# Performance work log

Measured on AMD Instinct MI355X. Metric: run time of the kernel, lower is better.

The kernel has to match this reference:

```python
import jax, jax.numpy as jnp
import numpy as np

N_NODES = 50000
N_EDGES = 800000
IN_C, HID_C, OUT_C = 128, 128, 64


def gcn_conv(x, src, dst, W, b, n_nodes):
    """PyG GCNConv: add self-loops, symmetric deg^-1/2 normalization,
    linear transform, scatter-add aggregation at target nodes, add bias."""
    # in-degree over (A + I), unit edge weights
    deg = jax.ops.segment_sum(jnp.ones(dst.shape[0], dtype=x.dtype), dst,
                              num_segments=n_nodes)
    dinv = jnp.where(deg > 0, jax.lax.rsqrt(deg), 0.0)
    norm = dinv[src] * dinv[dst]                      # [E+N]
    h = x @ W                                          # [N, out]
    msg = h[src] * norm[:, None]                       # gather + scale
    out = jax.ops.segment_sum(msg, dst, num_segments=n_nodes)  # scatter-add
    return out + b


def setup_inputs() -> dict:
    key = jax.random.key(0)
    k1, k2, k3, k4 = jax.random.split(key, 4)
    x = jax.random.normal(k1, (N_NODES, IN_C), dtype=jnp.float32)
    edge_index = jax.random.randint(k2, (2, N_EDGES), 0, N_NODES, dtype=jnp.int32)
    # Glorot-ish init for weights, zero bias (PyG default bias=True, zeros)
    W1 = jax.random.normal(k3, (IN_C, HID_C), dtype=jnp.float32) * (1.0 / np.sqrt(IN_C))
    b1 = jnp.zeros((HID_C,), dtype=jnp.float32)
    W2 = jax.random.normal(k4, (HID_C, OUT_C), dtype=jnp.float32) * (1.0 / np.sqrt(HID_C))
    b2 = jnp.zeros((OUT_C,), dtype=jnp.float32)
    return {"x": x, "edge_index": edge_index, "W1": W1, "b1": b1, "W2": W2, "b2": b2}


def reference(x, edge_index, W1, b1, W2, b2):
    n_nodes = x.shape[0]
    # add self-loops once (shared by both conv layers)
    loop = jnp.arange(n_nodes, dtype=edge_index.dtype)
    src = jnp.concatenate([edge_index[0], loop])
    dst = jnp.concatenate([edge_index[1], loop])
    h = gcn_conv(x, src, dst, W1, b1, n_nodes)
    h = jax.nn.relu(h)
    out = gcn_conv(h, src, dst, W2, b2, n_nodes)
    return out
```

## Files before the change

### kernel.cpp

```cpp
#include <hip/hip_runtime.h>
#include <hip/hip_fp16.h>


#define N_NODES 50000
#define N_EDGES 800000
#define BINW    128
#define NBIN    391
#define CAP     2560
#define CAP2    6656
#define B_CHUNK 2048
#define NB_SCAT ((N_EDGES + B_CHUNK - 1) / B_CHUNK)

typedef __bf16 bf16x8 __attribute__((ext_vector_type(8)));
typedef float  f32x4  __attribute__((ext_vector_type(4)));

template<int N>
__device__ inline void wprep_body(const float* __restrict__ W,
                                  __bf16* __restrict__ hi, __bf16* __restrict__ lo,
                                  int idx) {
    if (idx >= (N / 16) * 4 * 64) return;
    int l = idx & 63;
    int s = (idx >> 6) & 3;
    int c = idx >> 8;
    int n = c * 16 + (l & 15);
    int k0 = s * 32 + (l >> 4) * 8;
#pragma unroll
    for (int j = 0; j < 8; j++) {
        float w = W[(k0 + j) * N + n];
        __bf16 h = (__bf16)w;
        hi[idx * 8 + j] = h;
        lo[idx * 8 + j] = (__bf16)(w - (float)h);
    }
}

__global__ __launch_bounds__(256) void prep_kernel(
        const float* __restrict__ W1, const float* __restrict__ W2,
        __bf16* __restrict__ w1hi, __bf16* __restrict__ w1lo,
        __bf16* __restrict__ w2hi, __bf16* __restrict__ w2lo,
        int* __restrict__ gcur, __half* __restrict__ hs1, __half* __restrict__ hs2) {
    int b = blockIdx.x, tid = threadIdx.x;
    if (b < 8)       wprep_body<128>(W1, w1hi, w1lo, b * 256 + tid);
    else if (b < 12) wprep_body<64> (W2, w2hi, w2lo, (b - 8) * 256 + tid);
    else {
        for (int i = tid; i < NBIN; i += 256) gcur[i] = 0;
        if (tid < 128) hs1[(size_t)N_NODES * 128 + tid] = __float2half(0.f);
        if (tid < 64)  hs2[(size_t)N_NODES * 64 + tid] = __float2half(0.f);
    }
}


__global__ __launch_bounds__(256) void bin_scatter_kernel(
        const int* __restrict__ src, const int* __restrict__ dst,
        int* __restrict__ gcur, unsigned* __restrict__ ebin) {
    __shared__ int cnt[512];
    __shared__ int boff[512];
    __shared__ int bcur[512];
    __shared__ int gbase[512];
    __shared__ unsigned stage[B_CHUNK];
    __shared__ int ex[256];
    int tid = threadIdx.x;
    int e0 = blockIdx.x * B_CHUNK;

    cnt[tid] = 0; cnt[tid + 256] = 0;
    __syncthreads();

    unsigned key[8]; int bins[8];
#pragma unroll
    for (int i = 0; i < 8; i++) {
        int e = e0 + tid + i * 256;
        if (e < N_EDGES) {
            int d = dst[e], s = src[e];
            key[i]  = ((unsigned)d << 16) | (unsigned)s;
            bins[i] = d >> 7;
            atomicAdd(&cnt[bins[i]], 1);
        } else bins[i] = -1;
    }
    __syncthreads();

    int a = cnt[2 * tid], b = cnt[2 * tid + 1];
    ex[tid] = a + b;
    __syncthreads();
    for (int off = 1; off < 256; off <<= 1) {
        int t = (tid >= off) ? ex[tid - off] : 0;
        __syncthreads();
        ex[tid] += t;
        __syncthreads();
    }
    int myex = ex[tid] - (a + b);
    boff[2 * tid] = myex;     boff[2 * tid + 1] = myex + a;
    bcur[2 * tid] = myex;     bcur[2 * tid + 1] = myex + a;
    __syncthreads();

#pragma unroll
    for (int i = 0; i < 8; i++) {
        if (bins[i] >= 0) {
            int p = atomicAdd(&bcur[bins[i]], 1);
            stage[p] = key[i];
        }
    }

    __syncthreads();
    for (int b2 = tid; b2 < NBIN; b2 += 256) {
        int c = cnt[b2];
        gbase[b2] = (c > 0) ? atomicAdd(&gcur[b2], c) : 0;
    }
    __syncthreads();

    int total = N_EDGES - e0; if (total > B_CHUNK) total = B_CHUNK;
    for (int i = tid; i < total; i += 256) {
        unsigned k = stage[i];
        int bin = (int)(k >> 23);
        int idx = gbase[bin] + (i - boff[bin]);
        if (idx < CAP) ebin[(size_t)bin * CAP + idx] = k;
    }
}

__global__ __launch_bounds__(256) void bin_build_kernel(
        const unsigned* __restrict__ ebin, const int* __restrict__ gcur,
        int* __restrict__ deg, int* __restrict__ row_off,
        float* __restrict__ dinv, int* __restrict__ ssrc) {
    __shared__ int dl[BINW];
    __shared__ int pref[BINW];
    __shared__ int cur[BINW];
    __shared__ int padTotal;
    int bin = blockIdx.x, tid = threadIdx.x;
    if (tid < BINW) dl[tid] = 0;
    __syncthreads();
    int cnt = gcur[bin]; if (cnt > CAP) cnt = CAP;
    const unsigned* eb = ebin + (size_t)bin * CAP;
    for (int i = tid; i < cnt; i += 256)
        atomicAdd(&dl[(eb[i] >> 16) & 127], 1);
    __syncthreads();
    int pc = 0;
    if (tid < BINW) { pc = (dl[tid] + 15) & ~15; pref[tid] = pc; }
    __syncthreads();
    for (int off = 1; off < BINW; off <<= 1) {
        int t = 0;
        if (tid < BINW && tid >= off) t = pref[tid - off];
        __syncthreads();
        if (tid < BINW) pref[tid] += t;
        __syncthreads();
    }
    if (tid < BINW) {
        int ex = pref[tid] - pc;
        cur[tid] = ex;
        int node = bin * BINW + tid;
        if (node < N_NODES) {
            deg[node]     = dl[tid];
            row_off[node] = bin * CAP2 + ex;
            dinv[node]    = rsqrtf((float)(dl[tid] + 1));
        }
        if (tid == BINW - 1) padTotal = pref[tid];
    }
    __syncthreads();
    int pt4 = padTotal >> 2;
    int4* sb4 = (int4*)(ssrc + (size_t)bin * CAP2);
    int4 sent = make_int4(N_NODES, N_NODES, N_NODES, N_NODES);
    for (int i = tid; i < pt4; i += 256) sb4[i] = sent;
    __syncthreads();
    int* sb = ssrc + (size_t)bin * CAP2;
    for (int i = tid; i < cnt; i += 256) {
        unsigned k = eb[i];
        int p = atomicAdd(&cur[(k >> 16) & 127], 1);
        sb[p] = (int)(k & 0xFFFFu);
    }
}

__global__ __launch_bounds__(256) void gemm_mfma128_kernel(
        const float* __restrict__ X, const __bf16* __restrict__ Whi,
        const __bf16* __restrict__ Wlo, const float* __restrict__ dinv,
        __half* __restrict__ hs) {
    constexpr int NC = 8;
    int tid = threadIdx.x;
    int w = tid >> 6, lane = tid & 63;
    int q = lane >> 4, lr = lane & 15;
    int rb = blockIdx.x * 64 + w * 16;
    int row = rb + lr;
    int rowc = (row < N_NODES) ? row : (N_NODES - 1);

    f32x4 acc[NC];
#pragma unroll
    for (int c = 0; c < NC; c++) acc[c] = (f32x4){0.f, 0.f, 0.f, 0.f};

#pragma unroll
    for (int s = 0; s < 4; s++) {
        const float* xp = X + (size_t)rowc * 128 + s * 32 + q * 8;
        float4 x0 = *(const float4*)xp;
        float4 x1 = *(const float4*)(xp + 4);
        float xv[8] = {x0.x, x0.y, x0.z, x0.w, x1.x, x1.y, x1.z, x1.w};
        bf16x8 a_hi, a_lo;
#pragma unroll
        for (int j = 0; j < 8; j++) {
            __bf16 h = (__bf16)xv[j];
            a_hi[j] = h;
            a_lo[j] = (__bf16)(xv[j] - (float)h);
        }
#pragma unroll
        for (int c = 0; c < NC; c++) {
            size_t fo = (size_t)((c * 4 + s) * 64 + lane) * 8;
            bf16x8 bh = *(const bf16x8*)(Whi + fo);
            bf16x8 bl = *(const bf16x8*)(Wlo + fo);
            acc[c] = __builtin_amdgcn_mfma_f32_16x16x32_bf16(a_hi, bh, acc[c], 0, 0, 0);
            acc[c] = __builtin_amdgcn_mfma_f32_16x16x32_bf16(a_lo, bh, acc[c], 0, 0, 0);
            acc[c] = __builtin_amdgcn_mfma_f32_16x16x32_bf16(a_hi, bl, acc[c], 0, 0, 0);
        }
    }

#pragma unroll
    for (int r = 0; r < 4; r++) {
        int grow = rb + q * 4 + r;
        if (grow < N_NODES) {
            float sc = dinv[grow];
#pragma unroll
            for (int c = 0; c < NC; c++) {
                hs[(size_t)grow * 128 + c * 16 + lr] = __float2half(acc[c][r] * sc);
            }
        }
    }
}

__global__ __launch_bounds__(1024) void fused_agg_gemm_kernel(
        const __half* __restrict__ hs1, const int* __restrict__ row_off,
        const int* __restrict__ deg, const int* __restrict__ ssrc,
        const float* __restrict__ dinv, const float* __restrict__ bias,
        const __bf16* __restrict__ w2hi, const __bf16* __restrict__ w2lo,
        __half* __restrict__ hs2) {
    __shared__ float x2buf[16][132];
    int wave = threadIdx.x >> 6;
    int lane = threadIdx.x & 63;
    int rb = blockIdx.x * 16;
    int node = rb + wave;

    int beg = __builtin_amdgcn_readfirstlane(row_off[node]);
    int d   = __builtin_amdgcn_readfirstlane(deg[node]);
    float di = dinv[node];
    const char* Hb = (const char*)hs1;
    float ax = 0.f, ay = 0.f;

    for (int jj = 0; jj < d; jj += 64) {
        int s_all = ssrc[beg + jj + lane];
        int jend = d - jj; if (jend > 64) jend = 64;
#pragma unroll
        for (int b = 0; b < 4; b++) {
            if (b * 16 < jend) {
                unsigned vv[16];
#pragma unroll
                for (int u = 0; u < 16; u++) {
                    int su = __builtin_amdgcn_readlane(s_all, b * 16 + u);
                    vv[u] = *(const unsigned*)(Hb + (size_t)su * 256 + lane * 4);
                }
#pragma unroll
                for (int u = 0; u < 16; u++) {
                    float2 f = __half22float2(*(const __half2*)&vv[u]);
                    ax += f.x; ay += f.y;
                }
            }
        }
    }

    float2 sf = __half22float2(((const __half2*)(Hb + (size_t)node * 256))[lane]);
    float2 bb = ((const float2*)bias)[lane];
    float2 o;
    o.x = fmaxf(fmaf(di, ax + sf.x, bb.x), 0.f);
    o.y = fmaxf(fmaf(di, ay + sf.y, bb.y), 0.f);
    *(float2*)&x2buf[wave][2 * lane] = o;
    __syncthreads();

    if (threadIdx.x < 256) {
        int c = wave;
        int q = lane >> 4, lr = lane & 15;
        f32x4 g = (f32x4){0.f, 0.f, 0.f, 0.f};
#pragma unroll
        for (int s = 0; s < 4; s++) {
            const float* xp = &x2buf[lr][s * 32 + q * 8];
            float4 a0 = *(const float4*)xp;
            float4 a1 = *(const float4*)(xp + 4);
            float xv[8] = {a0.x, a0.y, a0.z, a0.w, a1.x, a1.y, a1.z, a1.w};
            bf16x8 a_hi, a_lo;
#pragma unroll
            for (int j = 0; j < 8; j++) {
                __bf16 h = (__bf16)xv[j];
                a_hi[j] = h;
                a_lo[j] = (__bf16)(xv[j] - (float)h);
            }
            size_t fo = (size_t)((c * 4 + s) * 64 + lane) * 8;
            bf16x8 bh = *(const bf16x8*)(w2hi + fo);
            bf16x8 bl = *(const bf16x8*)(w2lo + fo);
            g = __builtin_amdgcn_mfma_f32_16x16x32_bf16(a_hi, bh, g, 0, 0, 0);
            g = __builtin_amdgcn_mfma_f32_16x16x32_bf16(a_lo, bh, g, 0, 0, 0);
            g = __builtin_amdgcn_mfma_f32_16x16x32_bf16(a_hi, bl, g, 0, 0, 0);
        }
#pragma unroll
        for (int r = 0; r < 4; r++) {
            int grow = rb + q * 4 + r;
            hs2[(size_t)grow * 64 + c * 16 + lr] = __float2half(g[r] * dinv[grow]);
        }
    }
}

__global__ __launch_bounds__(256) void aggregate64_kernel(
        const __half* __restrict__ hs, const int* __restrict__ row_off,
        const int* __restrict__ deg, const int* __restrict__ ssrc,
        const float* __restrict__ dinv, const float* __restrict__ bias,
        float* __restrict__ out) {
    int node = (blockIdx.x * 256 + threadIdx.x) >> 6;
    int lane = threadIdx.x & 63;
    if (node >= N_NODES) return;
    int beg = __builtin_amdgcn_readfirstlane(row_off[node]);
    int d   = __builtin_amdgcn_readfirstlane(deg[node]);
    float di = dinv[node];
    const char* Hb = (const char*)hs;
    float acc = 0.f;

    for (int jj = 0; jj < d; jj += 64) {
        int s_all = ssrc[beg + jj + lane];
        int jend = d - jj; if (jend > 64) jend = 64;
#pragma unroll
        for (int b = 0; b < 4; b++) {
            if (b * 16 < jend) {
                unsigned short vv[16];
#pragma unroll
                for (int u = 0; u < 16; u++) {
                    int su = __builtin_amdgcn_readlane(s_all, b * 16 + u);
                    vv[u] = *(const unsigned short*)(Hb + (size_t)su * 128 + lane * 2);
                }
#pragma unroll
                for (int u = 0; u < 16; u++) {
                    acc += __half2float(*(const __half*)&vv[u]);
                }
            }
        }
    }

    float sf = __half2float(((const __half*)(Hb + (size_t)node * 128))[lane]);
    out[(size_t)node * 64 + lane] = fmaf(di, acc + sf, bias[lane]);
}


extern "C" void kernel_launch(void* const* d_in, const int* in_sizes, int n_in,
                              void* d_out, int out_size, void* d_ws, size_t ws_size,
                              hipStream_t stream) {
    const float* x  = (const float*)d_in[0];
    const int*   ei = (const int*)d_in[1];
    const float* W1 = (const float*)d_in[2];
    const float* b1 = (const float*)d_in[3];
    const float* W2 = (const float*)d_in[4];
    const float* b2 = (const float*)d_in[5];
    float* out = (float*)d_out;

    const int* src = ei;
    const int* dst = ei + N_EDGES;

    char* p = (char*)d_ws;
    size_t off = 0;
    auto alloc = [&](size_t bytes) { void* q = p + off; off += (bytes + 255) & ~(size_t)255; return q; };
    float*    dinv    = (float*)   alloc(N_NODES * 4);
    int*      deg     = (int*)     alloc(N_NODES * 4);
    int*      row_off = (int*)     alloc(N_NODES * 4);
    int*      gcur    = (int*)     alloc(NBIN * 4);
    int*      ssrc    = (int*)     alloc((size_t)NBIN * CAP2 * 4);
    unsigned* ebin    = (unsigned*)alloc((size_t)NBIN * CAP * 4);
    __bf16*   w1hi    = (__bf16*)  alloc(128 * 128 * 2);
    __bf16*   w1lo    = (__bf16*)  alloc(128 * 128 * 2);
    __bf16*   w2hi    = (__bf16*)  alloc(128 * 64 * 2);
    __bf16*   w2lo    = (__bf16*)  alloc(128 * 64 * 2);
    __half*   hs1     = (__half*)  alloc((size_t)(N_NODES + 1) * 128 * 2);
    __half*   hs2     = (__half*)  alloc((size_t)(N_NODES + 1) * 64 * 2);

    prep_kernel<<<13, 256, 0, stream>>>(W1, W2, w1hi, w1lo, w2hi, w2lo, gcur, hs1, hs2);
    bin_scatter_kernel<<<NB_SCAT, 256, 0, stream>>>(src, dst, gcur, ebin);
    bin_build_kernel<<<NBIN, 256, 0, stream>>>(ebin, gcur, deg, row_off, dinv, ssrc);

    gemm_mfma128_kernel<<<(N_NODES + 63) / 64, 256, 0, stream>>>(x, w1hi, w1lo, dinv, hs1);
    fused_agg_gemm_kernel<<<N_NODES / 16, 1024, 0, stream>>>(
        hs1, row_off, deg, ssrc, dinv, b1, w2hi, w2lo, hs2);
    aggregate64_kernel<<<(N_NODES * 64 + 255) / 256, 256, 0, stream>>>(
        hs2, row_off, deg, ssrc, dinv, b2, out);
}
```

Before: 175.0 us.

## Merge layer-1 GEMM with edge binning by deferring source dinv scaling

The layer-1 GEMM no longer multiplies rows by dinv, so it no longer depends on degree computation. It is merged into the bin-scatter launch as extra blocks that run concurrently with edge binning, and one kernel launch is removed. In exchange, the aggregation loop now loads dinv[src] for every neighbour and applies it with an FMA, with a sentinel dinv entry set to zero for padded slots. This adds per-edge gathers and stores unscaled fp16 values, which slightly changes rounding.

```diff
diff --git a/kernel.cpp b/kernel.cpp
--- a/kernel.cpp
+++ b/kernel.cpp
@@ -10,6 +10,7 @@
 #define CAP2    6656
 #define B_CHUNK 2048
 #define NB_SCAT ((N_EDGES + B_CHUNK - 1) / B_CHUNK)
+#define NB_GEMM ((N_NODES + 63) / 64)
 
 typedef __bf16 bf16x8 __attribute__((ext_vector_type(8)));
 typedef float  f32x4  __attribute__((ext_vector_type(4)));
@@ -37,7 +38,8 @@
         const float* __restrict__ W1, const float* __restrict__ W2,
         __bf16* __restrict__ w1hi, __bf16* __restrict__ w1lo,
         __bf16* __restrict__ w2hi, __bf16* __restrict__ w2lo,
-        int* __restrict__ gcur, __half* __restrict__ hs1, __half* __restrict__ hs2) {
+        int* __restrict__ gcur, __half* __restrict__ hs1, __half* __restrict__ hs2,
+        float* __restrict__ dinv) {
     int b = blockIdx.x, tid = threadIdx.x;
     if (b < 8)       wprep_body<128>(W1, w1hi, w1lo, b * 256 + tid);
     else if (b < 12) wprep_body<64> (W2, w2hi, w2lo, (b - 8) * 256 + tid);
@@ -45,11 +47,12 @@
         for (int i = tid; i < NBIN; i += 256) gcur[i] = 0;
         if (tid < 128) hs1[(size_t)N_NODES * 128 + tid] = __float2half(0.f);
         if (tid < 64)  hs2[(size_t)N_NODES * 64 + tid] = __float2half(0.f);
-    }
-}
-
-
-__global__ __launch_bounds__(256) void bin_scatter_kernel(
+        if (tid == 0)  dinv[N_NODES] = 0.f;
+    }
+}
+
+
+__device__ inline void bin_scatter_body(
         const int* __restrict__ src, const int* __restrict__ dst,
         int* __restrict__ gcur, unsigned* __restrict__ ebin) {
     __shared__ int cnt[512];
@@ -115,6 +118,66 @@
     }
 }
 
+__device__ inline void gemm_mfma128_body(
+        int gb, const float* __restrict__ X, const __bf16* __restrict__ Whi,
+        const __bf16* __restrict__ Wlo, __half* __restrict__ hs) {
+    constexpr int NC = 8;
+    int tid = threadIdx.x;
+    int w = tid >> 6, lane = tid & 63;
+    int q = lane >> 4, lr = lane & 15;
+    int rb = gb * 64 + w * 16;
+    int row = rb + lr;
+    int rowc = (row < N_NODES) ? row : (N_NODES - 1);
+
+    f32x4 acc[NC];
+#pragma unroll
+    for (int c = 0; c < NC; c++) acc[c] = (f32x4){0.f, 0.f, 0.f, 0.f};
+
+#pragma unroll
+    for (int s = 0; s < 4; s++) {
+        const float* xp = X + (size_t)rowc * 128 + s * 32 + q * 8;
+        float4 x0 = *(const float4*)xp;
+        float4 x1 = *(const float4*)(xp + 4);
+        float xv[8] = {x0.x, x0.y, x0.z, x0.w, x1.x, x1.y, x1.z, x1.w};
+        bf16x8 a_hi, a_lo;
+#pragma unroll
+        for (int j = 0; j < 8; j++) {
+            __bf16 h = (__bf16)xv[j];
+            a_hi[j] = h;
+            a_lo[j] = (__bf16)(xv[j] - (float)h);
+        }
+#pragma unroll
+        for (int c = 0; c < NC; c++) {
+            size_t fo = (size_t)((c * 4 + s) * 64 + lane) * 8;
+            bf16x8 bh = *(const bf16x8*)(Whi + fo);
+            bf16x8 bl = *(const bf16x8*)(Wlo + fo);
+            acc[c] = __builtin_amdgcn_mfma_f32_16x16x32_bf16(a_hi, bh, acc[c], 0, 0, 0);
+            acc[c] = __builtin_amdgcn_mfma_f32_16x16x32_bf16(a_lo, bh, acc[c], 0, 0, 0);
+            acc[c] = __builtin_amdgcn_mfma_f32_16x16x32_bf16(a_hi, bl, acc[c], 0, 0, 0);
+        }
+    }
+
+#pragma unroll
+    for (int r = 0; r < 4; r++) {
+        int grow = rb + q * 4 + r;
+        if (grow < N_NODES) {
+#pragma unroll
+            for (int c = 0; c < NC; c++) {
+                hs[(size_t)grow * 128 + c * 16 + lr] = __float2half(acc[c][r]);
+            }
+        }
+    }
+}
+
+__global__ __launch_bounds__(256) void scatter_gemm_kernel(
+        const int* __restrict__ src, const int* __restrict__ dst,
+        int* __restrict__ gcur, unsigned* __restrict__ ebin,
+        const float* __restrict__ X, const __bf16* __restrict__ Whi,
+        const __bf16* __restrict__ Wlo, __half* __restrict__ hs1) {
+    if (blockIdx.x < NB_SCAT) bin_scatter_body(src, dst, gcur, ebin);
+    else gemm_mfma128_body(blockIdx.x - NB_SCAT, X, Whi, Wlo, hs1);
+}
+
 __global__ __launch_bounds__(256) void bin_build_kernel(
         const unsigned* __restrict__ ebin, const int* __restrict__ gcur,
         int* __restrict__ deg, int* __restrict__ row_off,
@@ -163,59 +226,6 @@
         unsigned k = eb[i];
         int p = atomicAdd(&cur[(k >> 16) & 127], 1);
         sb[p] = (int)(k & 0xFFFFu);
-    }
-}
-
-__global__ __launch_bounds__(256) void gemm_mfma128_kernel(
-        const float* __restrict__ X, const __bf16* __restrict__ Whi,
-        const __bf16* __restrict__ Wlo, const float* __restrict__ dinv,
-        __half* __restrict__ hs) {
-    constexpr int NC = 8;
-    int tid = threadIdx.x;
-    int w = tid >> 6, lane = tid & 63;
-    int q = lane >> 4, lr = lane & 15;
-    int rb = blockIdx.x * 64 + w * 16;
-    int row = rb + lr;
-    int rowc = (row < N_NODES) ? row : (N_NODES - 1);
-
-    f32x4 acc[NC];
-#pragma unroll
-    for (int c = 0; c < NC; c++) acc[c] = (f32x4){0.f, 0.f, 0.f, 0.f};
-
-#pragma unroll
-    for (int s = 0; s < 4; s++) {
-        const float* xp = X + (size_t)rowc * 128 + s * 32 + q * 8;
-        float4 x0 = *(const float4*)xp;
-        float4 x1 = *(const float4*)(xp + 4);
-        float xv[8] = {x0.x, x0.y, x0.z, x0.w, x1.x, x1.y, x1.z, x1.w};
-        bf16x8 a_hi, a_lo;
-#pragma unroll
-        for (int j = 0; j < 8; j++) {
-            __bf16 h = (__bf16)xv[j];
-            a_hi[j] = h;
-            a_lo[j] = (__bf16)(xv[j] - (float)h);
-        }
-#pragma unroll
-        for (int c = 0; c < NC; c++) {
-            size_t fo = (size_t)((c * 4 + s) * 64 + lane) * 8;
-            bf16x8 bh = *(const bf16x8*)(Whi + fo);
-            bf16x8 bl = *(const bf16x8*)(Wlo + fo);
-            acc[c] = __builtin_amdgcn_mfma_f32_16x16x32_bf16(a_hi, bh, acc[c], 0, 0, 0);
-            acc[c] = __builtin_amdgcn_mfma_f32_16x16x32_bf16(a_lo, bh, acc[c], 0, 0, 0);
-            acc[c] = __builtin_amdgcn_mfma_f32_16x16x32_bf16(a_hi, bl, acc[c], 0, 0, 0);
-        }
-    }
-
-#pragma unroll
-    for (int r = 0; r < 4; r++) {
-        int grow = rb + q * 4 + r;
-        if (grow < N_NODES) {
-            float sc = dinv[grow];
-#pragma unroll
-            for (int c = 0; c < NC; c++) {
-                hs[(size_t)grow * 128 + c * 16 + lr] = __float2half(acc[c][r] * sc);
-            }
-        }
     }
 }
 
@@ -243,16 +253,18 @@
 #pragma unroll
         for (int b = 0; b < 4; b++) {
             if (b * 16 < jend) {
-                unsigned vv[16];
+                unsigned vv[16]; float ws[16];
 #pragma unroll
                 for (int u = 0; u < 16; u++) {
                     int su = __builtin_amdgcn_readlane(s_all, b * 16 + u);
                     vv[u] = *(const unsigned*)(Hb + (size_t)su * 256 + lane * 4);
+                    ws[u] = dinv[su];
                 }
 #pragma unroll
                 for (int u = 0; u < 16; u++) {
                     float2 f = __half22float2(*(const __half2*)&vv[u]);
-                    ax += f.x; ay += f.y;
+                    ax = fmaf(ws[u], f.x, ax);
+                    ay = fmaf(ws[u], f.y, ay);
                 }
             }
         }
@@ -260,9 +272,11 @@
 
     float2 sf = __half22float2(((const __half2*)(Hb + (size_t)node * 256))[lane]);
     float2 bb = ((const float2*)bias)[lane];
+    float tx = fmaf(di, sf.x, ax);
+    float ty = fmaf(di, sf.y, ay);
     float2 o;
-    o.x = fmaxf(fmaf(di, ax + sf.x, bb.x), 0.f);
-    o.y = fmaxf(fmaf(di, ay + sf.y, bb.y), 0.f);
+    o.x = fmaxf(fmaf(di, tx, bb.x), 0.f);
+    o.y = fmaxf(fmaf(di, ty, bb.y), 0.f);
     *(float2*)&x2buf[wave][2 * lane] = o;
     __syncthreads();
 
@@ -354,7 +368,7 @@
     char* p = (char*)d_ws;
     size_t off = 0;
     auto alloc = [&](size_t bytes) { void* q = p + off; off += (bytes + 255) & ~(size_t)255; return q; };
-    float*    dinv    = (float*)   alloc(N_NODES * 4);
+    float*    dinv    = (float*)   alloc((N_NODES + 1) * 4);
     int*      deg     = (int*)     alloc(N_NODES * 4);
     int*      row_off = (int*)     alloc(N_NODES * 4);
     int*      gcur    = (int*)     alloc(NBIN * 4);
@@ -367,11 +381,12 @@
     __half*   hs1     = (__half*)  alloc((size_t)(N_NODES + 1) * 128 * 2);
     __half*   hs2     = (__half*)  alloc((size_t)(N_NODES + 1) * 64 * 2);
 
-    prep_kernel<<<13, 256, 0, stream>>>(W1, W2, w1hi, w1lo, w2hi, w2lo, gcur, hs1, hs2);
-    bin_scatter_kernel<<<NB_SCAT, 256, 0, stream>>>(src, dst, gcur, ebin);
+    prep_kernel<<<13, 256, 0, stream>>>(W1, W2, w1hi, w1lo, w2hi, w2lo, gcur,
+                                        hs1, hs2, dinv);
+    scatter_gemm_kernel<<<NB_SCAT + NB_GEMM, 256, 0, stream>>>(
+        src, dst, gcur, ebin, x, w1hi, w1lo, hs1);
     bin_build_kernel<<<NBIN, 256, 0, stream>>>(ebin, gcur, deg, row_off, dinv, ssrc);
 
-    gemm_mfma128_kernel<<<(N_NODES + 63) / 64, 256, 0, stream>>>(x, w1hi, w1lo, dinv, hs1);
     fused_agg_gemm_kernel<<<N_NODES / 16, 1024, 0, stream>>>(
         hs1, row_off, deg, ssrc, dinv, b1, w2hi, w2lo, hs2);
     aggregate64_kernel<<<(N_NODES * 64 + 255) / 256, 256, 0, stream>>>(
```

Measured after the change: 168.9 us (median of 2 runs). 3.5% less time.
